# Optimization experiments

Measured on AMD Instinct MI355X. Metric: run time of the kernel, lower is better.

Reference implementation:

```python
import jax, jax.numpy as jnp
import numpy as np

B, S, C = 4, 4096, 1024
H, D, K = 16, 64, 256  # nhead, head_dim, dim_k


def setup_inputs() -> dict:
    key = jax.random.key(0)
    ks = jax.random.split(key, 7)
    x = jax.random.normal(ks[0], (B, S, C), dtype=jnp.float32)
    # per-head QKV projection weights (torch Linear weight layout [out,in])
    Wq = jax.random.normal(ks[1], (H, D, C), dtype=jnp.float32) * (C ** -0.5)
    Wk = jax.random.normal(ks[2], (H, D, C), dtype=jnp.float32) * (C ** -0.5)
    Wv = jax.random.normal(ks[3], (H, D, C), dtype=jnp.float32) * (C ** -0.5)
    # Linformer E/F sequence projections, per head: [K, S]
    We = jax.random.normal(ks[4], (H, K, S), dtype=jnp.float32) * (S ** -0.5)
    Wf = jax.random.normal(ks[5], (H, K, S), dtype=jnp.float32) * (S ** -0.5)
    # output projection (with bias, as w_o is nn.Linear default bias=True)
    Wo = jax.random.normal(ks[6], (C, H * D), dtype=jnp.float32) * ((H * D) ** -0.5)
    bo = jnp.zeros((C,), dtype=jnp.float32)
    return {"x": x, "Wq": Wq, "Wk": Wk, "Wv": Wv, "We": We, "Wf": Wf, "Wo": Wo, "bo": bo}


def reference(x, Wq, Wk, Wv, We, Wf, Wo, bo):
    # per-head projections: [B,H,S,D]
    Q = jnp.einsum('bsc,hdc->bhsd', x, Wq)
    Kh = jnp.einsum('bsc,hdc->bhsd', x, Wk)
    Vh = jnp.einsum('bsc,hdc->bhsd', x, Wv)
    # E-projection of K over the sequence axis: K^T [B,H,D,S] -> [B,H,D,K]
    Kp = jnp.einsum('bhsd,hks->bhdk', Kh, We)
    # scores: Q @ E(K^T) / sqrt(head_dim), softmax over low-rank axis k
    scale = 1.0 / jnp.sqrt(jnp.asarray(D, dtype=x.dtype))
    P = jax.nn.softmax(jnp.einsum('bhsd,bhdk->bhsk', Q, Kp) * scale, axis=-1)
    # F-projection of V over the sequence axis, then transpose back: [B,H,K,D]
    Vp = jnp.einsum('bhsd,hks->bhkd', Vh, Wf)
    out = jnp.einsum('bhsk,bhkd->bhsd', P, Vp)          # [B,H,S,D]
    out = out.transpose(0, 2, 1, 3).reshape(B, S, H * D)  # concat heads
    return jnp.einsum('bse,ce->bsc', out, Wo) + bo       # w_o (dropout=0)
```

## Files before the change

kernel.cpp:

```cpp
#include <hip/hip_runtime.h>
#include <stdint.h>


typedef unsigned short u16;
typedef __bf16 bf16t;
typedef bf16t bf16x8 __attribute__((ext_vector_type(8)));
typedef float f32x4 __attribute__((ext_vector_type(4)));
typedef u16 u16x8 __attribute__((ext_vector_type(8)));

#define MFMA16(a, b, c) __builtin_amdgcn_mfma_f32_16x16x32_bf16((a), (b), (c), 0, 0, 0)

__device__ __forceinline__ u16 f2bf(float f) {
  return __builtin_bit_cast(u16, (bf16t)f);
}

__device__ __forceinline__ bf16x8 ldf(const u16* p) { return *(const bf16x8*)p; }

__device__ __forceinline__ void gload16(const void* g, void* l) {
  __builtin_amdgcn_global_load_lds(
      (__attribute__((address_space(1))) void*)g,
      (__attribute__((address_space(3))) void*)l, 16, 0, 0);
}

__device__ __forceinline__ int xcd_swz(int orig, int nwg) {
  return (orig & 7) * (nwg >> 3) + (orig >> 3);
}

#define FENCE asm volatile("" ::: "memory")
#define BAR                                  \
  do {                                       \
    FENCE;                                   \
    __builtin_amdgcn_s_barrier();            \
    FENCE;                                   \
  } while (0)

__device__ __forceinline__ void gemm256_pipe(const u16* __restrict__ A,
                                             const u16* __restrict__ B,
                                             int m0, int n0, int sA1, int sB1,
                                             int s0, int kt0, f32x4 acc[8][4],
                                             char* smc) {
  const int tid = threadIdx.x;
  const int w = tid >> 6, l = tid & 63, g = l >> 4, r = l & 15;
  const int wr = w >> 2, wc = w & 3;
  const int lrow = l >> 2;
  const int ksw = (((l & 3) ^ ((l >> 3) & 3)) << 4);
  const int gx = ((g ^ ((r >> 1) & 3)) << 4);

  auto stage = [&](const u16* Base, int r0, int s1, int T, int ch, int ldsoff) {
#pragma unroll
    for (int i = 0; i < 2; ++i) {
      const int row = r0 + (w * 2 + i) * 16 + lrow;
      const size_t eoff = (size_t)(row >> 6) * s1 + (size_t)(row & 63) * s0;
      gload16((const char*)Base + eoff * 2 + ((kt0 + T) * 64 + ch * 32) * 2 + ksw,
              smc + ldsoff + (w * 2 + i) * 1024);
    }
  };

#define RD_B(dst, Bt)                                                     \
  _Pragma("unroll") for (int n = 0; n < 4; ++n)                           \
      dst[n] = *(const bf16x8*)((Bt) + (wc * 64 + n * 16 + r) * 64 + gx);
#define RD_A(dst, At, MH)                                                 \
  _Pragma("unroll") for (int m = 0; m < 4; ++m)                           \
      dst[m] = *(const bf16x8*)((At) + (wr * 128 + (MH)*64 + m * 16 + r) * 64 + gx);
#define QUAD(MH)                                                          \
  __builtin_amdgcn_s_setprio(1);                                          \
  _Pragma("unroll") for (int m = 0; m < 4; ++m)                           \
      _Pragma("unroll") for (int n = 0; n < 4; ++n)                       \
          acc[(MH)*4 + m][n] = MFMA16(af[m], bfv[n], acc[(MH)*4 + m][n]); \
  __builtin_amdgcn_s_setprio(0);

  stage(B, n0, sB1, 0, 0, 0 + 32768);
  stage(A, m0, sA1, 0, 0, 0 + 0);
  stage(B, n0, sB1, 0, 1, 0 + 49152);
  stage(A, m0, sA1, 0, 1, 0 + 16384);
  stage(B, n0, sB1, 1, 0, 65536 + 32768);
  stage(A, m0, sA1, 1, 0, 65536 + 0);
  stage(B, n0, sB1, 1, 1, 65536 + 49152);
  asm volatile("s_waitcnt vmcnt(10)" ::: "memory");
  BAR;

  for (int t = 0; t < 16; ++t) {
    const int buf = (t & 1) << 16, nb = buf ^ 65536;
    const int T1 = t < 15 ? t + 1 : 15;
    const int T2 = t < 14 ? t + 2 : 15;
    bf16x8 af[4], bfv[4];
    const char* At0 = smc + buf;
    const char* At1 = smc + buf + 16384;
    const char* Bt0 = smc + buf + 32768;
    const char* Bt1 = smc + buf + 49152;

    RD_B(bfv, Bt0)
    RD_A(af, At0, 0)
    stage(A, m0, sA1, T1, 1, nb + 16384);
    BAR;
    QUAD(0)
    BAR;
    RD_A(af, At0, 1)
    stage(B, n0, sB1, T2, 0, buf + 32768);
    asm volatile("s_waitcnt vmcnt(10)" ::: "memory");
    BAR;
    QUAD(1)
    BAR;
    RD_B(bfv, Bt1)
    RD_A(af, At1, 0)
    stage(A, m0, sA1, T2, 0, buf + 0);
    BAR;
    QUAD(0)
    BAR;
    RD_A(af, At1, 1)
    stage(B, n0, sB1, T2, 1, buf + 49152);
    asm volatile("s_waitcnt vmcnt(10)" ::: "memory");
    BAR;
    QUAD(1)
    BAR;
  }
#undef RD_B
#undef RD_A
#undef QUAD
}

__global__ __launch_bounds__(256) void cvt_all(
    const float* __restrict__ x, const float* __restrict__ Wq,
    const float* __restrict__ Wk, const float* __restrict__ Wv,
    const float* __restrict__ Wo, const float* __restrict__ We,
    const float* __restrict__ Wf, u16* __restrict__ xb, u16* __restrict__ wqkv,
    u16* __restrict__ wob, u16* __restrict__ web, u16* __restrict__ wfb) {
  const int i = blockIdx.x * 256 + threadIdx.x;
  const float* s;
  u16* d;
  int off;
  if (i < 2097152) {
    s = x; d = xb; off = i;
  } else if (i < 2621440) {
    const int j = i - 2097152, sel = j >> 17;
    off = j & 131071;
    if (sel == 0)      { s = Wq; d = wqkv; }
    else if (sel == 1) { s = Wk; d = wqkv + 1048576; }
    else if (sel == 2) { s = Wv; d = wqkv + 2097152; }
    else               { s = Wo; d = wob; }
  } else {
    const int j = i - 2621440;
    off = j & 2097151;
    if (j >> 21) { s = Wf; d = wfb; }
    else         { s = We; d = web; }
  }
  const size_t e = (size_t)off * 8;
  const float4 a = *(const float4*)(s + e);
  const float4 b = *(const float4*)(s + e + 4);
  u16x8 o;
  o[0] = f2bf(a.x); o[1] = f2bf(a.y); o[2] = f2bf(a.z); o[3] = f2bf(a.w);
  o[4] = f2bf(b.x); o[5] = f2bf(b.y); o[6] = f2bf(b.z); o[7] = f2bf(b.w);
  *(u16x8*)(d + e) = o;
}

__global__ __launch_bounds__(512, 2) void gemm_qkv(const u16* __restrict__ xb,
                                                   const u16* __restrict__ wqkv,
                                                   u16* __restrict__ Qd,
                                                   u16* __restrict__ KTd,
                                                   u16* __restrict__ VTd) {
  __shared__ u16 sm[65536];
  const int tid = threadIdx.x, w = tid >> 6, l = tid & 63, g = l >> 4, r = l & 15;
  const int wr = w >> 2, wc = w & 3;
  f32x4 acc[8][4] = {};
  if (blockIdx.x < 512) {
    const int wg = xcd_swz(blockIdx.x, 512);
    const int m0 = (wg & 7) * 256, n0 = (wg >> 3) * 256;
    gemm256_pipe(wqkv + 1048576, xb, m0, n0, 65536, 65536, 1024, 0, acc, (char*)sm);
#pragma unroll
    for (int m = 0; m < 8; ++m)
#pragma unroll
      for (int n = 0; n < 4; ++n)
#pragma unroll
        for (int j = 0; j < 4; ++j) {
          const int mm = m0 + wr * 128 + m * 16 + g * 4 + j;
          const int nn = n0 + wc * 64 + n * 16 + r;
          const int which = mm >> 10, hd = mm & 1023, h = hd >> 6, d = hd & 63;
          const int b = nn >> 12, s = nn & 4095;
          u16* dst = which ? VTd : KTd;
          dst[(((size_t)(b * 16 + h)) * 64 + d) * 4096 + s] = f2bf(acc[m][n][j]);
        }
  } else {
    const int wg = xcd_swz(blockIdx.x - 512, 256);
    const int m0 = (wg >> 2) * 256, n0 = (wg & 3) * 256;
    gemm256_pipe(xb, wqkv, m0, n0, 65536, 65536, 1024, 0, acc, (char*)sm);
#pragma unroll
    for (int m = 0; m < 8; ++m)
#pragma unroll
      for (int n = 0; n < 4; ++n)
#pragma unroll
        for (int j = 0; j < 4; ++j) {
          const int mm = m0 + wr * 128 + m * 16 + g * 4 + j;
          const int nn = n0 + wc * 64 + n * 16 + r;
          const int b = mm >> 12, s = mm & 4095, h = nn >> 6, d = nn & 63;
          Qd[(((size_t)(b * 16 + h)) * 4096 + s) * 64 + d] =
              f2bf(acc[m][n][j] * 0.125f);
        }
  }
}

__global__ __launch_bounds__(512, 2) void gemm_out(const u16* __restrict__ A,
                                                   const u16* __restrict__ BT,
                                                   const float* __restrict__ bo,
                                                   float* __restrict__ out) {
  __shared__ u16 sm[65536];
  const int wg = xcd_swz(blockIdx.x, 256);
  const int m0 = (wg >> 2) * 256, n0 = (wg & 3) * 256;
  const int tid = threadIdx.x, w = tid >> 6, l = tid & 63, g = l >> 4, r = l & 15;
  const int wr = w >> 2, wc = w & 3;
  f32x4 acc[8][4] = {};
  gemm256_pipe(A, BT, m0, n0, 65536, 65536, 1024, 0, acc, (char*)sm);
#pragma unroll
  for (int m = 0; m < 8; ++m)
#pragma unroll
    for (int n = 0; n < 4; ++n)
#pragma unroll
      for (int j = 0; j < 4; ++j) {
        const int mm = m0 + wr * 128 + m * 16 + g * 4 + j;
        const int nn = n0 + wc * 64 + n * 16 + r;
        out[(size_t)mm * 1024 + nn] = acc[m][n][j] + bo[nn];
      }
}

__global__ __launch_bounds__(512, 2) void gemm_small(const u16* __restrict__ web,
                                                     const u16* __restrict__ wfb,
                                                     const u16* __restrict__ KT,
                                                     const u16* __restrict__ VT,
                                                     float* __restrict__ part) {
  __shared__ u16 sm[65536];
  const int bx = blockIdx.x;
  const int h = bx & 15, mode = (bx >> 4) & 1, chunk = bx >> 5;
  const u16 *Ab, *Bb;
  int sA1, sB1;
  if (mode == 0) {
    Ab = web + (size_t)h * 1048576; sA1 = 262144;
    Bb = KT + (size_t)h * 262144;   sB1 = 4194304;
  } else {
    Ab = VT + (size_t)h * 262144;   sA1 = 4194304;
    Bb = wfb + (size_t)h * 1048576; sB1 = 262144;
  }
  f32x4 acc[8][4] = {};
  gemm256_pipe(Ab, Bb, 0, 0, sA1, sB1, 4096, chunk * 16, acc, (char*)sm);
  float* Cp = part + ((size_t)((mode * 4 + chunk) * 16 + h)) * 65536;
  const int tid = threadIdx.x, w = tid >> 6, l = tid & 63, g = l >> 4, r = l & 15;
  const int wr = w >> 2, wc = w & 3;
#pragma unroll
  for (int m = 0; m < 8; ++m)
#pragma unroll
    for (int n = 0; n < 4; ++n)
#pragma unroll
      for (int j = 0; j < 4; ++j)
        Cp[(size_t)(wr * 128 + m * 16 + g * 4 + j) * 256 + wc * 64 + n * 16 + r] =
            acc[m][n][j];
}

__global__ __launch_bounds__(256) void reduce_small(const float* __restrict__ part,
                                                    u16* __restrict__ Kp,
                                                    u16* __restrict__ VpT) {
  const int i = blockIdx.x * 256 + threadIdx.x;
  const int mode = i >> 18;
  const int rem = i & 262143;
  const int h = rem >> 14;
  const int e = (rem & 16383) * 4;
  const int m = e >> 8, n = e & 255;
  const float* pb = part + ((size_t)mode * 64 + h) * 65536 + e;
  const float4 s0 = *(const float4*)(pb);
  const float4 s1 = *(const float4*)(pb + 1048576);
  const float4 s2 = *(const float4*)(pb + 2097152);
  const float4 s3 = *(const float4*)(pb + 3145728);
  ushort4 o;
  o.x = f2bf(s0.x + s1.x + s2.x + s3.x);
  o.y = f2bf(s0.y + s1.y + s2.y + s3.y);
  o.z = f2bf(s0.z + s1.z + s2.z + s3.z);
  o.w = f2bf(s0.w + s1.w + s2.w + s3.w);
  if (mode == 0) {
    const int b = n >> 6, d = n & 63;
    *(ushort4*)(Kp + ((size_t)(b * 16 + h)) * 16384 + m * 64 + d) = o;
  } else {
    const int b = m >> 6, d = m & 63;
    *(ushort4*)(VpT + ((size_t)(b * 16 + h)) * 16384 + d * 256 + n) = o;
  }
}

__global__ __launch_bounds__(256, 1) void attn_fused(const u16* __restrict__ Q,
                                                     const u16* __restrict__ Kp,
                                                     const u16* __restrict__ VpT,
                                                     u16* __restrict__ att) {
  __shared__ u16 P[4][16 * 264];
  const int gid = blockIdx.x;
  const int bh = gid >> 3;
  const int st = gid & 7;
  const int hh = bh & 15, b = bh >> 4;
  const int tid = threadIdx.x, w = tid >> 6, l = tid & 63, g = l >> 4, r = l & 15;
  const u16* Kpb = Kp + (size_t)bh * 256 * 64;
  const u16* Vb = VpT + (size_t)bh * 64 * 256;

  bf16x8 kf[32];
  bf16x8 vf[32];
#pragma unroll
  for (int fn = 0; fn < 16; ++fn) {
    kf[fn * 2 + 0] = ldf(Kpb + (fn * 16 + r) * 64 + g * 8);
    kf[fn * 2 + 1] = ldf(Kpb + (fn * 16 + r) * 64 + 32 + g * 8);
  }
#pragma unroll
  for (int fn2 = 0; fn2 < 4; ++fn2)
#pragma unroll
    for (int kk = 0; kk < 8; ++kk)
      vf[fn2 * 8 + kk] = ldf(Vb + (fn2 * 16 + r) * 256 + kk * 32 + g * 8);

  u16* Pw = P[w];
  for (int t = 0; t < 8; ++t) {
    const int s0 = st * 512 + t * 64 + w * 16;
    const u16* Qb = Q + ((size_t)bh * 4096 + s0) * 64;
    const bf16x8 qf0 = ldf(Qb + r * 64 + g * 8);
    const bf16x8 qf1 = ldf(Qb + r * 64 + 32 + g * 8);
    f32x4 sc[16];
#pragma unroll
    for (int fn = 0; fn < 16; ++fn) {
      sc[fn] = MFMA16(qf0, kf[fn * 2 + 0], (f32x4){});
      sc[fn] = MFMA16(qf1, kf[fn * 2 + 1], sc[fn]);
    }
    float rinv[4];
#pragma unroll
    for (int j = 0; j < 4; ++j) {
      float sum = 0.f;
#pragma unroll
      for (int fn = 0; fn < 16; ++fn) {
        const float e = __expf(sc[fn][j]);
        sc[fn][j] = e;
        sum += e;
      }
      sum += __shfl_xor(sum, 1);
      sum += __shfl_xor(sum, 2);
      sum += __shfl_xor(sum, 4);
      sum += __shfl_xor(sum, 8);
      rinv[j] = 1.0f / sum;
    }
#pragma unroll
    for (int fn = 0; fn < 16; ++fn)
#pragma unroll
      for (int j = 0; j < 4; ++j)
        Pw[(g * 4 + j) * 264 + fn * 16 + r] = f2bf(sc[fn][j]);

    f32x4 o[4] = {};
#pragma unroll
    for (int kk = 0; kk < 8; ++kk) {
      const bf16x8 pa = ldf(Pw + r * 264 + kk * 32 + g * 8);
#pragma unroll
      for (int fn2 = 0; fn2 < 4; ++fn2)
        o[fn2] = MFMA16(pa, vf[fn2 * 8 + kk], o[fn2]);
    }
#pragma unroll
    for (int fn2 = 0; fn2 < 4; ++fn2)
#pragma unroll
      for (int j = 0; j < 4; ++j) {
        const int s = s0 + g * 4 + j;
        const int d = fn2 * 16 + r;
        att[((size_t)b * 4096 + s) * 1024 + hh * 64 + d] = f2bf(o[fn2][j] * rinv[j]);
      }
  }
}

extern "C" void kernel_launch(void* const* d_in, const int* in_sizes, int n_in,
                              void* d_out, int out_size, void* d_ws, size_t ws_size,
                              hipStream_t stream) {
  (void)in_sizes; (void)n_in; (void)out_size; (void)ws_size;
  const float* x  = (const float*)d_in[0];
  const float* Wq = (const float*)d_in[1];
  const float* Wk = (const float*)d_in[2];
  const float* Wv = (const float*)d_in[3];
  const float* We = (const float*)d_in[4];
  const float* Wf = (const float*)d_in[5];
  const float* Wo = (const float*)d_in[6];
  const float* bo = (const float*)d_in[7];
  char* ws = (char*)d_ws;
  u16* xb    = (u16*)(ws + 0);
  float* prt = (float*)(ws + 0);
  u16* att   = (u16*)(ws + 0);
  u16* wqkv  = (u16*)(ws + 33554432);
  u16* web   = (u16*)(ws + 39845888);
  u16* wfb   = (u16*)(ws + 73400320);
  u16* wob   = (u16*)(ws + 106954752);
  u16* Qd    = (u16*)(ws + 109051904);
  u16* KTd   = (u16*)(ws + 142606336);
  u16* VTd   = (u16*)(ws + 176160768);
  u16* Kpd   = (u16*)(ws + 209715200);
  u16* VpTd  = (u16*)(ws + 211812352);

  cvt_all<<<26624, 256, 0, stream>>>(x, Wq, Wk, Wv, Wo, We, Wf, xb, wqkv, wob,
                                     web, wfb);
  gemm_qkv<<<768, 512, 0, stream>>>(xb, wqkv, Qd, KTd, VTd);
  gemm_small<<<128, 512, 0, stream>>>(web, wfb, KTd, VTd, prt);
  reduce_small<<<2048, 256, 0, stream>>>(prt, Kpd, VpTd);
  attn_fused<<<512, 256, 0, stream>>>(Qd, Kpd, VpTd, att);
  gemm_out<<<256, 512, 0, stream>>>(att, wob, bo, (float*)d_out);
}
```

Before: 311.0 us.

## Fuse We/Wf fp32-to-bf16 conversion into sequence-projection GEMM and double split-K chunks

The separate conversion pass that wrote bf16 copies of the large We/Wf matrices is removed. gemm_small now loads fp32 We/Wf directly, converts them in registers and writes them into swizzled LDS alongside the async-loaded K/V tiles. The split-K factor rises from 4 to 8, giving 256 blocks instead of 128 for better CU occupancy, and reduce_small sums 8 partials. This removes a full write and reread of about 64MB of bf16 weights. In exchange, the new GEMM uses a simpler double-buffered pipeline with a full vmcnt(0) wait, and writes more partial-sum traffic.

```diff
diff --git a/kernel.cpp b/kernel.cpp
--- a/kernel.cpp
+++ b/kernel.cpp
@@ -122,27 +122,21 @@
 __global__ __launch_bounds__(256) void cvt_all(
     const float* __restrict__ x, const float* __restrict__ Wq,
     const float* __restrict__ Wk, const float* __restrict__ Wv,
-    const float* __restrict__ Wo, const float* __restrict__ We,
-    const float* __restrict__ Wf, u16* __restrict__ xb, u16* __restrict__ wqkv,
-    u16* __restrict__ wob, u16* __restrict__ web, u16* __restrict__ wfb) {
+    const float* __restrict__ Wo, u16* __restrict__ xb, u16* __restrict__ wqkv,
+    u16* __restrict__ wob) {
   const int i = blockIdx.x * 256 + threadIdx.x;
   const float* s;
   u16* d;
   int off;
   if (i < 2097152) {
     s = x; d = xb; off = i;
-  } else if (i < 2621440) {
+  } else {
     const int j = i - 2097152, sel = j >> 17;
     off = j & 131071;
     if (sel == 0)      { s = Wq; d = wqkv; }
     else if (sel == 1) { s = Wk; d = wqkv + 1048576; }
     else if (sel == 2) { s = Wv; d = wqkv + 2097152; }
     else               { s = Wo; d = wob; }
-  } else {
-    const int j = i - 2621440;
-    off = j & 2097151;
-    if (j >> 21) { s = Wf; d = wfb; }
-    else         { s = We; d = web; }
   }
   const size_t e = (size_t)off * 8;
   const float4 a = *(const float4*)(s + e);
@@ -221,28 +215,107 @@
       }
 }
 
-__global__ __launch_bounds__(512, 2) void gemm_small(const u16* __restrict__ web,
-                                                     const u16* __restrict__ wfb,
+__global__ __launch_bounds__(512, 2) void gemm_small(const float* __restrict__ WeF,
+                                                     const float* __restrict__ WfF,
                                                      const u16* __restrict__ KT,
                                                      const u16* __restrict__ VT,
                                                      float* __restrict__ part) {
   __shared__ u16 sm[65536];
+  char* smc = (char*)sm;
   const int bx = blockIdx.x;
   const int h = bx & 15, mode = (bx >> 4) & 1, chunk = bx >> 5;
-  const u16 *Ab, *Bb;
-  int sA1, sB1;
-  if (mode == 0) {
-    Ab = web + (size_t)h * 1048576; sA1 = 262144;
-    Bb = KT + (size_t)h * 262144;   sB1 = 4194304;
-  } else {
-    Ab = VT + (size_t)h * 262144;   sA1 = 4194304;
-    Bb = wfb + (size_t)h * 1048576; sB1 = 262144;
-  }
-  f32x4 acc[8][4] = {};
-  gemm256_pipe(Ab, Bb, 0, 0, sA1, sB1, 4096, chunk * 16, acc, (char*)sm);
-  float* Cp = part + ((size_t)((mode * 4 + chunk) * 16 + h)) * 65536;
+  const float* Wp = (mode == 0 ? WeF : WfF) + (size_t)h * 1048576;
+  const u16* Gp = (mode == 0 ? KT : VT) + (size_t)h * 262144;
   const int tid = threadIdx.x, w = tid >> 6, l = tid & 63, g = l >> 4, r = l & 15;
   const int wr = w >> 2, wc = w & 3;
+  const int xc = (tid & 7) ^ ((tid >> 3) & 7);
+  const int aR = tid >> 1;
+  const int aS0 = (tid & 1) * 4;
+
+  auto stageX = [&](int kt, int buf) {
+#pragma unroll
+    for (int i = 0; i < 4; ++i) {
+      const int row = i * 64 + (tid >> 3);
+      const int b = row >> 6, d = row & 63;
+      gload16(Gp + (size_t)b * 4194304 + (size_t)d * 4096 + kt * 64 + xc * 8,
+              smc + buf * 65536 + i * 8192 + tid * 16);
+    }
+  };
+  float4 aw[8];
+  auto loadY = [&](int kt) {
+#pragma unroll
+    for (int q = 0; q < 4; ++q) {
+      const float* p = Wp + (size_t)aR * 4096 + kt * 64 + (aS0 + q) * 8;
+      aw[q * 2 + 0] = *(const float4*)(p);
+      aw[q * 2 + 1] = *(const float4*)(p + 4);
+    }
+  };
+  auto writeY = [&](int buf) {
+#pragma unroll
+    for (int q = 0; q < 4; ++q) {
+      const float* f0 = (const float*)&aw[q * 2];
+      const float* f1 = (const float*)&aw[q * 2 + 1];
+      u16x8 o;
+#pragma unroll
+      for (int e = 0; e < 4; ++e) {
+        o[e] = f2bf(f0[e]);
+        o[e + 4] = f2bf(f1[e]);
+      }
+      *(u16x8*)(smc + buf * 65536 + 32768 + aR * 128 +
+                (((aS0 + q) ^ (aR & 7)) << 4)) = o;
+    }
+  };
+
+  f32x4 acc[8][4] = {};
+  auto compute = [&](int buf) {
+    const char* X = smc + buf * 65536;
+    const char* Y = X + 32768;
+    const char* Ar = (mode == 0) ? Y : X;
+    const char* Br = (mode == 0) ? X : Y;
+#pragma unroll
+    for (int kk = 0; kk < 2; ++kk) {
+      bf16x8 af[8], bfv[4];
+#pragma unroll
+      for (int n = 0; n < 4; ++n) {
+        const int row = wc * 64 + n * 16 + r;
+        bfv[n] = *(const bf16x8*)(Br + row * 128 + (((kk * 4 + g) ^ (r & 7)) << 4));
+      }
+#pragma unroll
+      for (int m = 0; m < 8; ++m) {
+        const int row = wr * 128 + m * 16 + r;
+        af[m] = *(const bf16x8*)(Ar + row * 128 + (((kk * 4 + g) ^ (r & 7)) << 4));
+      }
+      __builtin_amdgcn_s_setprio(1);
+#pragma unroll
+      for (int m = 0; m < 8; ++m)
+#pragma unroll
+        for (int n = 0; n < 4; ++n)
+          acc[m][n] = MFMA16(af[m], bfv[n], acc[m][n]);
+      __builtin_amdgcn_s_setprio(0);
+    }
+  };
+
+  const int kt0 = chunk * 8;
+  stageX(kt0, 0);
+  loadY(kt0);
+  asm volatile("s_waitcnt vmcnt(0)" ::: "memory");
+  writeY(0);
+  __syncthreads();
+  for (int t = 0; t < 8; ++t) {
+    const int buf = t & 1;
+    if (t < 7) {
+      stageX(kt0 + t + 1, buf ^ 1);
+      loadY(kt0 + t + 1);
+    }
+    compute(buf);
+    if (t < 7) {
+      asm volatile("s_waitcnt vmcnt(0)" ::: "memory");
+      writeY(buf ^ 1);
+    }
+    __syncthreads();
+  }
+
+  float* Cp = part + ((size_t)((mode * 8 + chunk) * 16 + h)) * 65536;
 #pragma unroll
   for (int m = 0; m < 8; ++m)
 #pragma unroll
@@ -262,16 +335,15 @@
   const int h = rem >> 14;
   const int e = (rem & 16383) * 4;
   const int m = e >> 8, n = e & 255;
-  const float* pb = part + ((size_t)mode * 64 + h) * 65536 + e;
-  const float4 s0 = *(const float4*)(pb);
-  const float4 s1 = *(const float4*)(pb + 1048576);
-  const float4 s2 = *(const float4*)(pb + 2097152);
-  const float4 s3 = *(const float4*)(pb + 3145728);
+  const float* pb = part + ((size_t)mode * 128 + h) * 65536 + e;
+  float4 acc = *(const float4*)(pb);
+#pragma unroll
+  for (int c = 1; c < 8; ++c) {
+    const float4 s = *(const float4*)(pb + (size_t)c * 1048576);
+    acc.x += s.x; acc.y += s.y; acc.z += s.z; acc.w += s.w;
+  }
   ushort4 o;
-  o.x = f2bf(s0.x + s1.x + s2.x + s3.x);
-  o.y = f2bf(s0.y + s1.y + s2.y + s3.y);
-  o.z = f2bf(s0.z + s1.z + s2.z + s3.z);
-  o.w = f2bf(s0.w + s1.w + s2.w + s3.w);
+  o.x = f2bf(acc.x); o.y = f2bf(acc.y); o.z = f2bf(acc.z); o.w = f2bf(acc.w);
   if (mode == 0) {
     const int b = n >> 6, d = n & 63;
     *(ushort4*)(Kp + ((size_t)(b * 16 + h)) * 16384 + m * 64 + d) = o;
@@ -375,10 +447,8 @@
   char* ws = (char*)d_ws;
   u16* xb    = (u16*)(ws + 0);
   float* prt = (float*)(ws + 0);
-  u16* att   = (u16*)(ws + 0);
   u16* wqkv  = (u16*)(ws + 33554432);
-  u16* web   = (u16*)(ws + 39845888);
-  u16* wfb   = (u16*)(ws + 73400320);
+  u16* att   = (u16*)(ws + 73400320);
   u16* wob   = (u16*)(ws + 106954752);
   u16* Qd    = (u16*)(ws + 109051904);
   u16* KTd   = (u16*)(ws + 142606336);
@@ -386,10 +456,9 @@
   u16* Kpd   = (u16*)(ws + 209715200);
   u16* VpTd  = (u16*)(ws + 211812352);
 
-  cvt_all<<<26624, 256, 0, stream>>>(x, Wq, Wk, Wv, Wo, We, Wf, xb, wqkv, wob,
-                                     web, wfb);
+  cvt_all<<<10240, 256, 0, stream>>>(x, Wq, Wk, Wv, Wo, xb, wqkv, wob);
   gemm_qkv<<<768, 512, 0, stream>>>(xb, wqkv, Qd, KTd, VTd);
-  gemm_small<<<128, 512, 0, stream>>>(web, wfb, KTd, VTd, prt);
+  gemm_small<<<256, 512, 0, stream>>>(We, Wf, KTd, VTd, prt);
   reduce_small<<<2048, 256, 0, stream>>>(prt, Kpd, VpTd);
   attn_fused<<<512, 256, 0, stream>>>(Qd, Kpd, VpTd, att);
   gemm_out<<<256, 512, 0, stream>>>(att, wob, bo, (float*)d_out);
```

Result: no change. 307.7 us (median of 3 runs) (-1.1%).
